# Optimization experiments

Measured on AMD Instinct MI355X. Metric: run time of the kernel, lower is better.

The kernel has to match this reference:

```python
import jax, jax.numpy as jnp
import numpy as np

N_NODES = 100000
N_EDGES = 1600000
N_FEAT = 512
HEADS = 8
F_HEAD = 8
HIDDEN = HEADS * F_HEAD  # 64
N_CLASSES = 40
NEG_SLOPE = 0.2


def setup_inputs() -> dict:
    key = jax.random.key(0)
    ks = jax.random.split(key, 10)
    x = jax.random.normal(ks[0], (N_NODES, N_FEAT), dtype=jnp.float32)
    edge_index = jax.random.randint(ks[1], (2, N_EDGES), 0, N_NODES, dtype=jnp.int32)
    s1 = 1.0 / np.sqrt(N_FEAT)
    s2 = 1.0 / np.sqrt(HIDDEN)
    return {
        "x": x,
        "edge_index": edge_index,
        "W1": jax.random.normal(ks[2], (N_FEAT, HIDDEN), dtype=jnp.float32) * s1,
        "att_src1": jax.random.normal(ks[3], (HEADS, F_HEAD), dtype=jnp.float32) * 0.1,
        "att_dst1": jax.random.normal(ks[4], (HEADS, F_HEAD), dtype=jnp.float32) * 0.1,
        "b1": jnp.zeros((HIDDEN,), dtype=jnp.float32),
        "W2": jax.random.normal(ks[5], (HIDDEN, N_CLASSES), dtype=jnp.float32) * s2,
        "att_src2": jax.random.normal(ks[6], (1, N_CLASSES), dtype=jnp.float32) * 0.1,
        "att_dst2": jax.random.normal(ks[7], (1, N_CLASSES), dtype=jnp.float32) * 0.1,
        "b2": jnp.zeros((N_CLASSES,), dtype=jnp.float32),
    }


def _gat_conv(x, src, dst, W, att_src, att_dst, bias, heads, f_out, concat):
    """PyG GATConv (v1). src/dst already include self-loops.
    x: [N, F_in]; W: [F_in, heads*f_out]; att_*: [heads, f_out]; bias: [heads*f_out] or [f_out]."""
    N = x.shape[0]
    h = (x @ W).reshape(N, heads, f_out)              # [N, H, F]
    a_src = jnp.sum(h * att_src[None], axis=-1)        # [N, H]
    a_dst = jnp.sum(h * att_dst[None], axis=-1)        # [N, H]
    e = jax.nn.leaky_relu(a_src[src] + a_dst[dst], NEG_SLOPE)  # [E, H]
    # segment softmax over incoming edges per destination node
    m = jax.ops.segment_max(e, dst, num_segments=N)    # [N, H]
    ex = jnp.exp(e - m[dst])
    denom = jax.ops.segment_sum(ex, dst, num_segments=N)
    alpha = ex / (denom[dst] + 1e-16)                  # [E, H]
    msg = h[src] * alpha[:, :, None]                   # [E, H, F]
    out = jax.ops.segment_sum(msg, dst, num_segments=N)  # [N, H, F]
    if concat:
        out = out.reshape(N, heads * f_out)
    else:
        out = out.mean(axis=1)
    return out + bias


def reference(x, edge_index, W1, att_src1, att_dst1, b1, W2, att_src2, att_dst2, b2):
    N = x.shape[0]
    loops = jnp.arange(N, dtype=edge_index.dtype)
    src = jnp.concatenate([edge_index[0], loops])
    dst = jnp.concatenate([edge_index[1], loops])
    # dropout layers are identity in eval mode
    h = _gat_conv(x, src, dst, W1, att_src1, att_dst1, b1, HEADS, F_HEAD, True)
    h = jax.nn.elu(h)
    out = _gat_conv(h, src, dst, W2, att_src2, att_dst2, b2, 1, N_CLASSES, False)
    return out
```

## Files before the change

### kernel.cpp

```cpp
#include <hip/hip_runtime.h>
#include <math.h>

#define N_NODES   100000
#define N_EDGES   1600000
#define E_TOT     (N_EDGES + N_NODES)
#define N_FEAT    512
#define HEADS     8
#define F_HEAD    8
#define HIDDEN    64
#define N_CLASSES 40

#define BSHIFT    9
#define NBUCK     196
#define SC_NBLK   256
#define SC_CHUNK  ((E_TOT + SC_NBLK - 1) / SC_NBLK)

#define CT        5

typedef __attribute__((ext_vector_type(8))) short short8_t;
typedef __attribute__((ext_vector_type(4))) float f32x4;
typedef _Float16 half_t;
typedef __attribute__((ext_vector_type(8))) _Float16 h16x8;

__device__ inline void f2bf2(float x, unsigned short& h, unsigned short& l) {
  union { float f; unsigned u; } a; a.f = x;
  unsigned rh = a.u + 0x7FFFu + ((a.u >> 16) & 1u);
  unsigned short hv = (unsigned short)(rh >> 16);
  union { unsigned u; float f; } hf; hf.u = ((unsigned)hv) << 16;
  union { float f; unsigned u; } b; b.f = x - hf.f;
  unsigned rl = b.u + 0x7FFFu + ((b.u >> 16) & 1u);
  h = hv;
  l = (unsigned short)(rl >> 16);
}

__device__ inline void cvt8(const float4& v0, const float4& v1, short8_t& hi, short8_t& lo) {
  float v[8] = {v0.x, v0.y, v0.z, v0.w, v1.x, v1.y, v1.z, v1.w};
#pragma unroll
  for (int e = 0; e < 8; ++e) {
    unsigned short hh, ll;
    f2bf2(v[e], hh, ll);
    hi[e] = (short)hh;
    lo[e] = (short)ll;
  }
}


__global__ __launch_bounds__(256) void k_bhist(const int* __restrict__ ei,
                                               int* __restrict__ ghT) {
  __shared__ int h[NBUCK];
  int b = blockIdx.x, t = threadIdx.x;
  for (int i = t; i < NBUCK; i += 256) h[i] = 0;
  __syncthreads();
  int e0 = b * SC_CHUNK;
  int e1 = e0 + SC_CHUNK; if (e1 > E_TOT) e1 = E_TOT;
  for (int e = e0 + t; e < e1; e += 256) {
    int dst = (e < N_EDGES) ? ei[N_EDGES + e] : (e - N_EDGES);
    atomicAdd(&h[dst >> BSHIFT], 1);
  }
  __syncthreads();
  for (int i = t; i < NBUCK; i += 256) ghT[i * SC_NBLK + b] = h[i];
}

__global__ __launch_bounds__(256) void k_scan1(int* __restrict__ ghT,
                                               int* __restrict__ btot) {
  __shared__ int red[256];
  int k = blockIdx.x, t = threadIdx.x;
  int v = ghT[k * SC_NBLK + t];
  red[t] = v;
  __syncthreads();
  for (int off = 1; off < 256; off <<= 1) {
    int add = (t >= off) ? red[t - off] : 0;
    __syncthreads();
    red[t] += add;
    __syncthreads();
  }
  ghT[k * SC_NBLK + t] = red[t] - v;
  if (t == 255) btot[k] = red[255];
}

__global__ __launch_bounds__(256) void k_scan2(const int* __restrict__ btot,
                                               int* __restrict__ bbase) {
  __shared__ int red[256];
  int t = threadIdx.x;
  int v = (t < NBUCK) ? btot[t] : 0;
  red[t] = v;
  __syncthreads();
  for (int off = 1; off < 256; off <<= 1) {
    int add = (t >= off) ? red[t - off] : 0;
    __syncthreads();
    red[t] += add;
    __syncthreads();
  }
  if (t < NBUCK) bbase[t] = red[t] - v;
  if (t == NBUCK - 1) bbase[NBUCK] = red[t];
}

__global__ __launch_bounds__(256) void k_bscatter(const int* __restrict__ ei,
                                                  const int* __restrict__ ghT,
                                                  const int* __restrict__ bbase,
                                                  unsigned* __restrict__ ebuf) {
  __shared__ int offs[256];
  __shared__ int cnt[256];
  int b = blockIdx.x, t = threadIdx.x;
  offs[t] = (t < NBUCK) ? (ghT[t * SC_NBLK + b] + bbase[t]) : 0;
  cnt[t] = 0;
  __syncthreads();
  int e0 = b * SC_CHUNK;
  int e1 = e0 + SC_CHUNK; if (e1 > E_TOT) e1 = E_TOT;
  for (int e = e0 + t; e < e1; e += 256) {
    int src, dst;
    if (e < N_EDGES) { src = ei[e]; dst = ei[N_EDGES + e]; }
    else             { src = e - N_EDGES; dst = src; }
    int k = dst >> BSHIFT;
    int r = atomicAdd(&cnt[k], 1);
    ebuf[offs[k] + r] = (unsigned)src | ((unsigned)(dst & 511) << 17);
  }
}

__global__ __launch_bounds__(256) void k_fine(const unsigned* __restrict__ ebuf,
                                              const int* __restrict__ bbase,
                                              int* __restrict__ rowp,
                                              int* __restrict__ ssrc) {
  __shared__ int cnt[512];
  __shared__ int red[256];
  __shared__ int cur[512];
  int k = blockIdx.x, t = threadIdx.x;
  int base = bbase[k], end = bbase[k + 1];
  cnt[t] = 0; cnt[t + 256] = 0;
  __syncthreads();
  for (int i = base + t; i < end; i += 256) atomicAdd(&cnt[ebuf[i] >> 17], 1);
  __syncthreads();
  int c0 = cnt[2 * t], c1 = cnt[2 * t + 1];
  int s = c0 + c1;
  red[t] = s;
  __syncthreads();
  for (int off = 1; off < 256; off <<= 1) {
    int add = (t >= off) ? red[t - off] : 0;
    __syncthreads();
    red[t] += add;
    __syncthreads();
  }
  int excl = red[t] - s;
  int p0 = base + excl;
  int p1 = p0 + c0;
  cur[2 * t] = p0; cur[2 * t + 1] = p1;
  int node = (k << BSHIFT) + 2 * t;
  if (node < N_NODES)     rowp[node]     = p0;
  if (node + 1 < N_NODES) rowp[node + 1] = p1;
  if (k == NBUCK - 1 && t == 0) rowp[N_NODES] = E_TOT;
  __syncthreads();
  for (int i = base + t; i < end; i += 256) {
    unsigned p = ebuf[i];
    int pos = atomicAdd(&cur[p >> 17], 1);
    ssrc[pos] = (int)(p & 0x1FFFFu);
  }
}


__global__ void k_wprep(const float* __restrict__ W1, const float* __restrict__ att_src1,
                        const float* __restrict__ att_dst1, short* __restrict__ w1fh,
                        short* __restrict__ w1fl) {
  int idx = blockIdx.x * blockDim.x + threadIdx.x;
  if (idx < N_FEAT * HIDDEN) {
    int e    = idx & 7;
    int lane = (idx >> 3) & 63;
    int ct   = (idx >> 9) & 3;
    int ks   = idx >> 11;
    int col = ct * 16 + (lane & 15);
    int k   = ks * 32 + (lane >> 4) * 8 + e;
    unsigned short h, l;
    f2bf2(W1[k * HIDDEN + col], h, l);
    int didx = ((ks * CT + ct) * 64 + lane) * 8 + e;
    w1fh[didx] = (short)h;
    w1fl[didx] = (short)l;
  } else if (idx < N_FEAT * HIDDEN + N_FEAT * 16) {
    int i2 = idx - N_FEAT * HIDDEN;
    int c = i2 & 15;
    int k = i2 >> 4;
    int cc = c & 7;
    const float* att = (c < 8) ? att_src1 : att_dst1;
    float v = 0.f;
#pragma unroll
    for (int f = 0; f < 8; ++f) v = fmaf(W1[k * HIDDEN + cc * 8 + f], att[cc * 8 + f], v);
    unsigned short h, l;
    f2bf2(v, h, l);
    int lane = ((k >> 3) & 3) * 16 + c;
    int ks = k >> 5, e = k & 7;
    int didx = ((ks * CT + 4) * 64 + lane) * 8 + e;
    w1fh[didx] = (short)h;
    w1fl[didx] = (short)l;
  }
}


__global__ __launch_bounds__(256) void k_gemm1(const float* __restrict__ x,
                                               const short* __restrict__ w1fh,
                                               const short* __restrict__ w1fl,
                                               half_t* __restrict__ h1h,
                                               half_t* __restrict__ a_srch,
                                               float* __restrict__ a_dst1) {
  int t = threadIdx.x;
  int w = t >> 6, l = t & 63;
  int n0 = blockIdx.x * 128 + w * 32;
  int r0 = l & 15;
  int kq8 = (l >> 4) * 8;
  const float* pA = x + (size_t)(n0 + r0) * N_FEAT + kq8;
  const float* pB = x + (size_t)(n0 + 16 + r0) * N_FEAT + kq8;
  bool vA = (n0 + r0) < N_NODES;
  bool vB = (n0 + 16 + r0) < N_NODES;

  f32x4 acc[2][CT];
#pragma unroll
  for (int i = 0; i < 2; ++i)
#pragma unroll
    for (int j = 0; j < CT; ++j) acc[i][j] = (f32x4){0.f, 0.f, 0.f, 0.f};

#pragma unroll 2
  for (int gks = 0; gks < 16; ++gks) {
    int boff = gks * (CT * 512) + l * 8;
    short8_t bh[CT], bl[CT];
#pragma unroll
    for (int ct = 0; ct < CT; ++ct) {
      bh[ct] = *(const short8_t*)(w1fh + boff + ct * 512);
      bl[ct] = *(const short8_t*)(w1fl + boff + ct * 512);
    }
    float4 a0 = make_float4(0.f, 0.f, 0.f, 0.f), a1 = a0, c0 = a0, c1 = a0;
    if (vA) {
      const float4* p = (const float4*)(pA + gks * 32);
      a0 = p[0]; a1 = p[1];
    }
    if (vB) {
      const float4* p = (const float4*)(pB + gks * 32);
      c0 = p[0]; c1 = p[1];
    }
    short8_t ahA, alA, ahB, alB;
    cvt8(a0, a1, ahA, alA);
    cvt8(c0, c1, ahB, alB);
#pragma unroll
    for (int ct = 0; ct < CT; ++ct) {
      acc[0][ct] = __builtin_amdgcn_mfma_f32_16x16x32_bf16(ahA, bh[ct], acc[0][ct], 0, 0, 0);
      acc[0][ct] = __builtin_amdgcn_mfma_f32_16x16x32_bf16(ahA, bl[ct], acc[0][ct], 0, 0, 0);
      acc[0][ct] = __builtin_amdgcn_mfma_f32_16x16x32_bf16(alA, bh[ct], acc[0][ct], 0, 0, 0);
      acc[1][ct] = __builtin_amdgcn_mfma_f32_16x16x32_bf16(ahB, bh[ct], acc[1][ct], 0, 0, 0);
      acc[1][ct] = __builtin_amdgcn_mfma_f32_16x16x32_bf16(ahB, bl[ct], acc[1][ct], 0, 0, 0);
      acc[1][ct] = __builtin_amdgcn_mfma_f32_16x16x32_bf16(alB, bh[ct], acc[1][ct], 0, 0, 0);
    }
  }
#pragma unroll
  for (int rtl = 0; rtl < 2; ++rtl) {
    int rbase = n0 + rtl * 16 + (l >> 4) * 4;
    int col0 = l & 15;
#pragma unroll
    for (int ct = 0; ct < 4; ++ct) {
      int col = ct * 16 + col0;
#pragma unroll
      for (int r = 0; r < 4; ++r) {
        int node = rbase + r;
        if (node < N_NODES) h1h[(size_t)node * HIDDEN + col] = (half_t)acc[rtl][ct][r];
      }
    }
#pragma unroll
    for (int r = 0; r < 4; ++r) {
      int node = rbase + r;
      if (node < N_NODES) {
        float v = acc[rtl][4][r];
        if (col0 < 8) a_srch[(size_t)node * 8 + col0] = (half_t)v;
        else          a_dst1[(size_t)node * 8 + (col0 - 8)] = v;
      }
    }
  }
}


__global__ __launch_bounds__(256) void k_edge1(const int* __restrict__ rowp,
                                               const int* __restrict__ ssrc,
                                               const half_t* __restrict__ a_srch,
                                               const float* __restrict__ a_dst,
                                               const half_t* __restrict__ h1h,
                                               const float* __restrict__ b1,
                                               const float* __restrict__ W2,
                                               const float* __restrict__ att_src2,
                                               const float* __restrict__ att_dst2,
                                               half_t* __restrict__ h2h,
                                               float* __restrict__ a_src2,
                                               float* __restrict__ a_dst2) {
  __shared__ __align__(16) float w2s[HIDDEN * N_CLASSES];
  __shared__ float as2s[N_CLASSES], ad2s[N_CLASSES];
  __shared__ half_t exsh[4][64 * 9];
  __shared__ int   srcs[4][64];
  __shared__ float orow[4][64];
  int t = threadIdx.x;
  for (int i = t; i < HIDDEN * N_CLASSES; i += 256) w2s[i] = W2[i];
  if (t < N_CLASSES) { as2s[t] = att_src2[t]; ad2s[t] = att_dst2[t]; }
  __syncthreads();

  int wv = t >> 6, lane = t & 63;
  int node = __builtin_amdgcn_readfirstlane(blockIdx.x * 4 + wv);
  int s0 = __builtin_amdgcn_readfirstlane(rowp[node]);
  int s1 = __builtin_amdgcn_readfirstlane(rowp[node + 1]);

  float ad[8];
  {
    float4 d0 = *(const float4*)(a_dst + (size_t)node * 8);
    float4 d1 = *(const float4*)(a_dst + (size_t)node * 8 + 4);
    ad[0] = d0.x; ad[1] = d0.y; ad[2] = d0.z; ad[3] = d0.w;
    ad[4] = d1.x; ad[5] = d1.y; ad[6] = d1.z; ad[7] = d1.w;
  }
  float ac0 = 0.f, ac1 = 0.f, ac2 = 0.f, ac3 = 0.f;
  float ds0 = 0.f, ds1 = 0.f, ds2 = 0.f, ds3 = 0.f;
  int hof = lane >> 3;

  for (int base = s0; base < s1; base += 64) {
    int cn = s1 - base;
    cn = cn > 64 ? 64 : cn;
    asm volatile("" ::: "memory");
    if (lane < cn) {
      int sid = ssrc[base + lane];
      h16x8 Av = *(const h16x8*)(a_srch + (size_t)sid * 8);
      srcs[wv][lane] = sid;
#pragma unroll
      for (int h = 0; h < 8; ++h) {
        float e = (float)Av[h] + ad[h];
        e = e > 0.f ? e : 0.2f * e;
        exsh[wv][lane * 9 + h] = (half_t)__expf(e);
      }
    }
    asm volatile("s_waitcnt lgkmcnt(0)" ::: "memory");
    int j = 0;
    for (; j + 8 <= cn; j += 8) {
      float e0 = (float)exsh[wv][j * 9 + hof];
      float e1 = (float)exsh[wv][(j + 1) * 9 + hof];
      float e2 = (float)exsh[wv][(j + 2) * 9 + hof];
      float e3 = (float)exsh[wv][(j + 3) * 9 + hof];
      float e4 = (float)exsh[wv][(j + 4) * 9 + hof];
      float e5 = (float)exsh[wv][(j + 5) * 9 + hof];
      float e6 = (float)exsh[wv][(j + 6) * 9 + hof];
      float e7 = (float)exsh[wv][(j + 7) * 9 + hof];
      int sj0 = __builtin_amdgcn_readfirstlane(srcs[wv][j]);
      int sj1 = __builtin_amdgcn_readfirstlane(srcs[wv][j + 1]);
      int sj2 = __builtin_amdgcn_readfirstlane(srcs[wv][j + 2]);
      int sj3 = __builtin_amdgcn_readfirstlane(srcs[wv][j + 3]);
      int sj4 = __builtin_amdgcn_readfirstlane(srcs[wv][j + 4]);
      int sj5 = __builtin_amdgcn_readfirstlane(srcs[wv][j + 5]);
      int sj6 = __builtin_amdgcn_readfirstlane(srcs[wv][j + 6]);
      int sj7 = __builtin_amdgcn_readfirstlane(srcs[wv][j + 7]);
      float g0 = (float)(h1h + (size_t)sj0 * HIDDEN)[lane];
      float g1 = (float)(h1h + (size_t)sj1 * HIDDEN)[lane];
      float g2 = (float)(h1h + (size_t)sj2 * HIDDEN)[lane];
      float g3 = (float)(h1h + (size_t)sj3 * HIDDEN)[lane];
      float g4 = (float)(h1h + (size_t)sj4 * HIDDEN)[lane];
      float g5 = (float)(h1h + (size_t)sj5 * HIDDEN)[lane];
      float g6 = (float)(h1h + (size_t)sj6 * HIDDEN)[lane];
      float g7 = (float)(h1h + (size_t)sj7 * HIDDEN)[lane];
      ac0 = fmaf(e0, g0, ac0);  ds0 += e0;
      ac1 = fmaf(e1, g1, ac1);  ds1 += e1;
      ac2 = fmaf(e2, g2, ac2);  ds2 += e2;
      ac3 = fmaf(e3, g3, ac3);  ds3 += e3;
      ac0 = fmaf(e4, g4, ac0);  ds0 += e4;
      ac1 = fmaf(e5, g5, ac1);  ds1 += e5;
      ac2 = fmaf(e6, g6, ac2);  ds2 += e6;
      ac3 = fmaf(e7, g7, ac3);  ds3 += e7;
    }
    for (; j + 4 <= cn; j += 4) {
      float e0 = (float)exsh[wv][j * 9 + hof];
      float e1 = (float)exsh[wv][(j + 1) * 9 + hof];
      float e2 = (float)exsh[wv][(j + 2) * 9 + hof];
      float e3 = (float)exsh[wv][(j + 3) * 9 + hof];
      int sj0 = __builtin_amdgcn_readfirstlane(srcs[wv][j]);
      int sj1 = __builtin_amdgcn_readfirstlane(srcs[wv][j + 1]);
      int sj2 = __builtin_amdgcn_readfirstlane(srcs[wv][j + 2]);
      int sj3 = __builtin_amdgcn_readfirstlane(srcs[wv][j + 3]);
      float g0 = (float)(h1h + (size_t)sj0 * HIDDEN)[lane];
      float g1 = (float)(h1h + (size_t)sj1 * HIDDEN)[lane];
      float g2 = (float)(h1h + (size_t)sj2 * HIDDEN)[lane];
      float g3 = (float)(h1h + (size_t)sj3 * HIDDEN)[lane];
      ac0 = fmaf(e0, g0, ac0);  ds0 += e0;
      ac1 = fmaf(e1, g1, ac1);  ds1 += e1;
      ac2 = fmaf(e2, g2, ac2);  ds2 += e2;
      ac3 = fmaf(e3, g3, ac3);  ds3 += e3;
    }
    for (; j < cn; ++j) {
      float e0 = (float)exsh[wv][j * 9 + hof];
      int sj0 = __builtin_amdgcn_readfirstlane(srcs[wv][j]);
      ac0 = fmaf(e0, (float)(h1h + (size_t)sj0 * HIDDEN)[lane], ac0);
      ds0 += e0;
    }
  }
  float accv = (ac0 + ac1) + (ac2 + ac3);
  float dsum = (ds0 + ds1) + (ds2 + ds3);
  float o = accv / (dsum + 1e-16f);
  o += b1[lane];
  o = o > 0.f ? o : expm1f(o);
  orow[wv][lane] = o;
  asm volatile("s_waitcnt lgkmcnt(0)" ::: "memory");

  float hacc = 0.f;
  if (lane < N_CLASSES) {
#pragma unroll 16
    for (int k = 0; k < HIDDEN; ++k)
      hacc = fmaf(orow[wv][k], w2s[k * N_CLASSES + lane], hacc);
  }
  float pas = (lane < N_CLASSES) ? hacc * as2s[lane] : 0.f;
  float pad = (lane < N_CLASSES) ? hacc * ad2s[lane] : 0.f;
#pragma unroll
  for (int off = 1; off < 64; off <<= 1) {
    pas += __shfl_xor(pas, off);
    pad += __shfl_xor(pad, off);
  }
  if (lane < N_CLASSES) h2h[(size_t)node * N_CLASSES + lane] = (half_t)hacc;
  if (lane == 0) { a_src2[node] = pas; a_dst2[node] = pad; }
}


__global__ __launch_bounds__(256) void k_edge2(const int* __restrict__ rowp,
                                               const int* __restrict__ ssrc,
                                               const float* __restrict__ a_src,
                                               const float* __restrict__ a_dst,
                                               const half_t* __restrict__ h2h,
                                               const float* __restrict__ b2,
                                               float* __restrict__ out) {
  __shared__ float exs[4][64];
  __shared__ int   srcs[4][64];
  int t = threadIdx.x;
  int wv = t >> 6, lane = t & 63;
  int node = __builtin_amdgcn_readfirstlane(blockIdx.x * 4 + wv);
  int s0 = __builtin_amdgcn_readfirstlane(rowp[node]);
  int s1 = __builtin_amdgcn_readfirstlane(rowp[node + 1]);

  float adv = a_dst[node];
  float ac0 = 0.f, ac1 = 0.f, ac2 = 0.f, ac3 = 0.f;
  float ds0 = 0.f, ds1 = 0.f, ds2 = 0.f, ds3 = 0.f;
  bool act = lane < N_CLASSES;

  for (int base = s0; base < s1; base += 64) {
    int cn = s1 - base;
    cn = cn > 64 ? 64 : cn;
    asm volatile("" ::: "memory");
    if (lane < cn) {
      int sid = ssrc[base + lane];
      float e = a_src[sid] + adv;
      e = e > 0.f ? e : 0.2f * e;
      srcs[wv][lane] = sid;
      exs[wv][lane] = __expf(e);
    }
    asm volatile("s_waitcnt lgkmcnt(0)" ::: "memory");
    int j = 0;
    for (; j + 8 <= cn; j += 8) {
      float e0 = exs[wv][j],     e1 = exs[wv][j + 1];
      float e2 = exs[wv][j + 2], e3 = exs[wv][j + 3];
      float e4 = exs[wv][j + 4], e5 = exs[wv][j + 5];
      float e6 = exs[wv][j + 6], e7 = exs[wv][j + 7];
      int sj0 = __builtin_amdgcn_readfirstlane(srcs[wv][j]);
      int sj1 = __builtin_amdgcn_readfirstlane(srcs[wv][j + 1]);
      int sj2 = __builtin_amdgcn_readfirstlane(srcs[wv][j + 2]);
      int sj3 = __builtin_amdgcn_readfirstlane(srcs[wv][j + 3]);
      int sj4 = __builtin_amdgcn_readfirstlane(srcs[wv][j + 4]);
      int sj5 = __builtin_amdgcn_readfirstlane(srcs[wv][j + 5]);
      int sj6 = __builtin_amdgcn_readfirstlane(srcs[wv][j + 6]);
      int sj7 = __builtin_amdgcn_readfirstlane(srcs[wv][j + 7]);
      ds0 += e0; ds1 += e1; ds2 += e2; ds3 += e3;
      ds0 += e4; ds1 += e5; ds2 += e6; ds3 += e7;
      if (act) {
        float g0 = (float)(h2h + (size_t)sj0 * N_CLASSES)[lane];
        float g1 = (float)(h2h + (size_t)sj1 * N_CLASSES)[lane];
        float g2 = (float)(h2h + (size_t)sj2 * N_CLASSES)[lane];
        float g3 = (float)(h2h + (size_t)sj3 * N_CLASSES)[lane];
        float g4 = (float)(h2h + (size_t)sj4 * N_CLASSES)[lane];
        float g5 = (float)(h2h + (size_t)sj5 * N_CLASSES)[lane];
        float g6 = (float)(h2h + (size_t)sj6 * N_CLASSES)[lane];
        float g7 = (float)(h2h + (size_t)sj7 * N_CLASSES)[lane];
        ac0 = fmaf(e0, g0, ac0); ac1 = fmaf(e1, g1, ac1);
        ac2 = fmaf(e2, g2, ac2); ac3 = fmaf(e3, g3, ac3);
        ac0 = fmaf(e4, g4, ac0); ac1 = fmaf(e5, g5, ac1);
        ac2 = fmaf(e6, g6, ac2); ac3 = fmaf(e7, g7, ac3);
      }
    }
    for (; j < cn; ++j) {
      float e0 = exs[wv][j];
      int sj0 = __builtin_amdgcn_readfirstlane(srcs[wv][j]);
      ds0 += e0;
      if (act) ac0 = fmaf(e0, (float)(h2h + (size_t)sj0 * N_CLASSES)[lane], ac0);
    }
  }
  float accv = (ac0 + ac1) + (ac2 + ac3);
  float dsum = (ds0 + ds1) + (ds2 + ds3);
  if (act)
    out[(size_t)node * N_CLASSES + lane] = accv / (dsum + 1e-16f) + b2[lane];
}


extern "C" void kernel_launch(void* const* d_in, const int* in_sizes, int n_in,
                              void* d_out, int out_size, void* d_ws, size_t ws_size,
                              hipStream_t stream) {
  const float* x        = (const float*)d_in[0];
  const int*   ei       = (const int*)d_in[1];
  const float* W1       = (const float*)d_in[2];
  const float* att_src1 = (const float*)d_in[3];
  const float* att_dst1 = (const float*)d_in[4];
  const float* b1       = (const float*)d_in[5];
  const float* W2       = (const float*)d_in[6];
  const float* att_src2 = (const float*)d_in[7];
  const float* att_dst2 = (const float*)d_in[8];
  const float* b2       = (const float*)d_in[9];
  float* out = (float*)d_out;

  char* w = (char*)d_ws;
  half_t* h1h    = (half_t*)(w);
  half_t* h2h    = (half_t*)(w + 12800000);
  half_t* a_srch = (half_t*)(w + 20800000);
  float* a_dst1  = (float*)(w + 22400000);
  int*   rowp    = (int*)(w + 25600000);
  int*   ssrc    = (int*)(w + 26000128);
  short* w1fh    = (short*)(w + 32800128);
  short* w1fl    = (short*)(w + 32882048);
  float* a_src2  = (float*)(w + 32964096);
  float* a_dst2  = (float*)(w + 33364096);
  int*   btot    = (int*)(w + 33764096);
  int*   bbase   = (int*)(w + 33765120);
  unsigned* ebuf = (unsigned*)(w);
  int*   ghT     = (int*)(w + 12800000);

  k_wprep<<<(N_FEAT * HIDDEN + N_FEAT * 16 + 255) / 256, 256, 0, stream>>>(
      W1, att_src1, att_dst1, w1fh, w1fl);
  k_bhist<<<SC_NBLK, 256, 0, stream>>>(ei, ghT);
  k_scan1<<<NBUCK, 256, 0, stream>>>(ghT, btot);
  k_scan2<<<1, 256, 0, stream>>>(btot, bbase);
  k_bscatter<<<SC_NBLK, 256, 0, stream>>>(ei, ghT, bbase, ebuf);
  k_fine<<<NBUCK, 256, 0, stream>>>(ebuf, bbase, rowp, ssrc);

  k_gemm1<<<(N_NODES + 127) / 128, 256, 0, stream>>>(x, w1fh, w1fl, h1h, a_srch, a_dst1);
  k_edge1<<<N_NODES / 4, 256, 0, stream>>>(rowp, ssrc, a_srch, a_dst1, h1h, b1,
                                           W2, att_src2, att_dst2, h2h, a_src2, a_dst2);

  k_edge2<<<N_NODES / 4, 256, 0, stream>>>(rowp, ssrc, a_src2, a_dst2, h2h, b2, out);
}
```

Before: 290.7 us.

## Split layer-1 aggregation per head and move second GEMM into separate kernel

The fused edge-aggregation plus W2 projection kernel is split in two. A per-head aggregation kernel uses one wave per (node, head) pair, with lanes covering 8 edges by 8 features. A separate per-node GEMM2 kernel then computes h2 and the layer-2 attention scalars from an fp16 intermediate buffer. The aim is more parallelism and more gathers in flight during aggregation. The cost is 8x redundant reads of edge indices and attention logits, narrower 16-byte scattered gathers, an extra intermediate write and read, and one more kernel launch.

```diff
diff --git a/kernel.cpp b/kernel.cpp
--- a/kernel.cpp
+++ b/kernel.cpp
@@ -272,12 +272,70 @@
 }
 
 
-__global__ __launch_bounds__(256) void k_edge1(const int* __restrict__ rowp,
-                                               const int* __restrict__ ssrc,
-                                               const half_t* __restrict__ a_srch,
-                                               const float* __restrict__ a_dst,
-                                               const half_t* __restrict__ h1h,
-                                               const float* __restrict__ b1,
+__global__ __launch_bounds__(256) void k_edge1h(const int* __restrict__ rowp,
+                                                const int* __restrict__ ssrc,
+                                                const half_t* __restrict__ a_srch,
+                                                const float* __restrict__ a_dst1,
+                                                const half_t* __restrict__ h1h,
+                                                const float* __restrict__ b1,
+                                                half_t* __restrict__ out1h) {
+  __shared__ float exs[4][64];
+  __shared__ int   srcs[4][64];
+  int t = threadIdx.x;
+  int wv = t >> 6, lane = t & 63;
+  int head = blockIdx.x & 7;
+  int nb   = blockIdx.x >> 3;
+  int node = __builtin_amdgcn_readfirstlane(nb * 4 + wv);
+  int s0 = __builtin_amdgcn_readfirstlane(rowp[node]);
+  int s1 = __builtin_amdgcn_readfirstlane(rowp[node + 1]);
+  int es = lane >> 3, cg = lane & 7;
+  float adh = a_dst1[node * 8 + head];
+  const half_t* hbase = h1h + head * 8 + cg;
+
+  float ac0 = 0.f, ac1 = 0.f, ds0 = 0.f, ds1 = 0.f;
+
+  for (int base = s0; base < s1; base += 64) {
+    int cn = s1 - base;
+    cn = cn > 64 ? 64 : cn;
+    asm volatile("" ::: "memory");
+    int sid = 0;
+    float ex = 0.f;
+    if (lane < cn) {
+      sid = ssrc[base + lane];
+      float e = (float)a_srch[(size_t)sid * 8 + head] + adh;
+      e = e > 0.f ? e : 0.2f * e;
+      ex = __expf(e);
+    }
+    srcs[wv][lane] = sid;
+    exs[wv][lane] = ex;
+    asm volatile("s_waitcnt lgkmcnt(0)" ::: "memory");
+#pragma unroll
+    for (int jj = 0; jj < 8; jj += 2) {
+      int i0 = jj * 8 + es;
+      int i1 = i0 + 8;
+      int sj0 = srcs[wv][i0];
+      int sj1 = srcs[wv][i1];
+      float e0 = exs[wv][i0];
+      float e1 = exs[wv][i1];
+      float g0 = (float)hbase[(size_t)sj0 * HIDDEN];
+      float g1 = (float)hbase[(size_t)sj1 * HIDDEN];
+      ac0 = fmaf(e0, g0, ac0);  ds0 += e0;
+      ac1 = fmaf(e1, g1, ac1);  ds1 += e1;
+    }
+  }
+  float acc = ac0 + ac1;
+  float dsum = ds0 + ds1;
+  acc += __shfl_xor(acc, 8);  acc += __shfl_xor(acc, 16);  acc += __shfl_xor(acc, 32);
+  dsum += __shfl_xor(dsum, 8); dsum += __shfl_xor(dsum, 16); dsum += __shfl_xor(dsum, 32);
+  if (es == 0) {
+    float o = acc / (dsum + 1e-16f) + b1[head * 8 + cg];
+    o = o > 0.f ? o : expm1f(o);
+    out1h[(size_t)node * HIDDEN + head * 8 + cg] = (half_t)o;
+  }
+}
+
+
+__global__ __launch_bounds__(256) void k_gemm2(const half_t* __restrict__ out1h,
                                                const float* __restrict__ W2,
                                                const float* __restrict__ att_src2,
                                                const float* __restrict__ att_dst2,
@@ -285,130 +343,44 @@
                                                float* __restrict__ a_src2,
                                                float* __restrict__ a_dst2) {
   __shared__ __align__(16) float w2s[HIDDEN * N_CLASSES];
-  __shared__ float as2s[N_CLASSES], ad2s[N_CLASSES];
-  __shared__ half_t exsh[4][64 * 9];
-  __shared__ int   srcs[4][64];
-  __shared__ float orow[4][64];
+  __shared__ float as2[N_CLASSES], ad2[N_CLASSES];
   int t = threadIdx.x;
   for (int i = t; i < HIDDEN * N_CLASSES; i += 256) w2s[i] = W2[i];
-  if (t < N_CLASSES) { as2s[t] = att_src2[t]; ad2s[t] = att_dst2[t]; }
-  __syncthreads();
-
-  int wv = t >> 6, lane = t & 63;
-  int node = __builtin_amdgcn_readfirstlane(blockIdx.x * 4 + wv);
-  int s0 = __builtin_amdgcn_readfirstlane(rowp[node]);
-  int s1 = __builtin_amdgcn_readfirstlane(rowp[node + 1]);
-
-  float ad[8];
-  {
-    float4 d0 = *(const float4*)(a_dst + (size_t)node * 8);
-    float4 d1 = *(const float4*)(a_dst + (size_t)node * 8 + 4);
-    ad[0] = d0.x; ad[1] = d0.y; ad[2] = d0.z; ad[3] = d0.w;
-    ad[4] = d1.x; ad[5] = d1.y; ad[6] = d1.z; ad[7] = d1.w;
-  }
-  float ac0 = 0.f, ac1 = 0.f, ac2 = 0.f, ac3 = 0.f;
-  float ds0 = 0.f, ds1 = 0.f, ds2 = 0.f, ds3 = 0.f;
-  int hof = lane >> 3;
-
-  for (int base = s0; base < s1; base += 64) {
-    int cn = s1 - base;
-    cn = cn > 64 ? 64 : cn;
-    asm volatile("" ::: "memory");
-    if (lane < cn) {
-      int sid = ssrc[base + lane];
-      h16x8 Av = *(const h16x8*)(a_srch + (size_t)sid * 8);
-      srcs[wv][lane] = sid;
-#pragma unroll
-      for (int h = 0; h < 8; ++h) {
-        float e = (float)Av[h] + ad[h];
-        e = e > 0.f ? e : 0.2f * e;
-        exsh[wv][lane * 9 + h] = (half_t)__expf(e);
+  if (t < N_CLASSES) { as2[t] = att_src2[t]; ad2[t] = att_dst2[t]; }
+  __syncthreads();
+  int node = blockIdx.x * 256 + t;
+  if (node >= N_NODES) return;
+  const h16x8* rp = (const h16x8*)(out1h + (size_t)node * HIDDEN);
+  float acc[N_CLASSES];
+#pragma unroll
+  for (int c = 0; c < N_CLASSES; ++c) acc[c] = 0.f;
+  for (int k8 = 0; k8 < 8; ++k8) {
+    h16x8 rv = rp[k8];
+#pragma unroll
+    for (int kk = 0; kk < 8; ++kk) {
+      float r = (float)rv[kk];
+      const float* wrow = &w2s[(k8 * 8 + kk) * N_CLASSES];
+#pragma unroll
+      for (int c4 = 0; c4 < 10; ++c4) {
+        float4 wvv = *(const float4*)(wrow + c4 * 4);
+        acc[c4 * 4 + 0] = fmaf(r, wvv.x, acc[c4 * 4 + 0]);
+        acc[c4 * 4 + 1] = fmaf(r, wvv.y, acc[c4 * 4 + 1]);
+        acc[c4 * 4 + 2] = fmaf(r, wvv.z, acc[c4 * 4 + 2]);
+        acc[c4 * 4 + 3] = fmaf(r, wvv.w, acc[c4 * 4 + 3]);
       }
     }
-    asm volatile("s_waitcnt lgkmcnt(0)" ::: "memory");
-    int j = 0;
-    for (; j + 8 <= cn; j += 8) {
-      float e0 = (float)exsh[wv][j * 9 + hof];
-      float e1 = (float)exsh[wv][(j + 1) * 9 + hof];
-      float e2 = (float)exsh[wv][(j + 2) * 9 + hof];
-      float e3 = (float)exsh[wv][(j + 3) * 9 + hof];
-      float e4 = (float)exsh[wv][(j + 4) * 9 + hof];
-      float e5 = (float)exsh[wv][(j + 5) * 9 + hof];
-      float e6 = (float)exsh[wv][(j + 6) * 9 + hof];
-      float e7 = (float)exsh[wv][(j + 7) * 9 + hof];
-      int sj0 = __builtin_amdgcn_readfirstlane(srcs[wv][j]);
-      int sj1 = __builtin_amdgcn_readfirstlane(srcs[wv][j + 1]);
-      int sj2 = __builtin_amdgcn_readfirstlane(srcs[wv][j + 2]);
-      int sj3 = __builtin_amdgcn_readfirstlane(srcs[wv][j + 3]);
-      int sj4 = __builtin_amdgcn_readfirstlane(srcs[wv][j + 4]);
-      int sj5 = __builtin_amdgcn_readfirstlane(srcs[wv][j + 5]);
-      int sj6 = __builtin_amdgcn_readfirstlane(srcs[wv][j + 6]);
-      int sj7 = __builtin_amdgcn_readfirstlane(srcs[wv][j + 7]);
-      float g0 = (float)(h1h + (size_t)sj0 * HIDDEN)[lane];
-      float g1 = (float)(h1h + (size_t)sj1 * HIDDEN)[lane];
-      float g2 = (float)(h1h + (size_t)sj2 * HIDDEN)[lane];
-      float g3 = (float)(h1h + (size_t)sj3 * HIDDEN)[lane];
-      float g4 = (float)(h1h + (size_t)sj4 * HIDDEN)[lane];
-      float g5 = (float)(h1h + (size_t)sj5 * HIDDEN)[lane];
-      float g6 = (float)(h1h + (size_t)sj6 * HIDDEN)[lane];
-      float g7 = (float)(h1h + (size_t)sj7 * HIDDEN)[lane];
-      ac0 = fmaf(e0, g0, ac0);  ds0 += e0;
-      ac1 = fmaf(e1, g1, ac1);  ds1 += e1;
-      ac2 = fmaf(e2, g2, ac2);  ds2 += e2;
-      ac3 = fmaf(e3, g3, ac3);  ds3 += e3;
-      ac0 = fmaf(e4, g4, ac0);  ds0 += e4;
-      ac1 = fmaf(e5, g5, ac1);  ds1 += e5;
-      ac2 = fmaf(e6, g6, ac2);  ds2 += e6;
-      ac3 = fmaf(e7, g7, ac3);  ds3 += e7;
-    }
-    for (; j + 4 <= cn; j += 4) {
-      float e0 = (float)exsh[wv][j * 9 + hof];
-      float e1 = (float)exsh[wv][(j + 1) * 9 + hof];
-      float e2 = (float)exsh[wv][(j + 2) * 9 + hof];
-      float e3 = (float)exsh[wv][(j + 3) * 9 + hof];
-      int sj0 = __builtin_amdgcn_readfirstlane(srcs[wv][j]);
-      int sj1 = __builtin_amdgcn_readfirstlane(srcs[wv][j + 1]);
-      int sj2 = __builtin_amdgcn_readfirstlane(srcs[wv][j + 2]);
-      int sj3 = __builtin_amdgcn_readfirstlane(srcs[wv][j + 3]);
-      float g0 = (float)(h1h + (size_t)sj0 * HIDDEN)[lane];
-      float g1 = (float)(h1h + (size_t)sj1 * HIDDEN)[lane];
-      float g2 = (float)(h1h + (size_t)sj2 * HIDDEN)[lane];
-      float g3 = (float)(h1h + (size_t)sj3 * HIDDEN)[lane];
-      ac0 = fmaf(e0, g0, ac0);  ds0 += e0;
-      ac1 = fmaf(e1, g1, ac1);  ds1 += e1;
-      ac2 = fmaf(e2, g2, ac2);  ds2 += e2;
-      ac3 = fmaf(e3, g3, ac3);  ds3 += e3;
-    }
-    for (; j < cn; ++j) {
-      float e0 = (float)exsh[wv][j * 9 + hof];
-      int sj0 = __builtin_amdgcn_readfirstlane(srcs[wv][j]);
-      ac0 = fmaf(e0, (float)(h1h + (size_t)sj0 * HIDDEN)[lane], ac0);
-      ds0 += e0;
-    }
-  }
-  float accv = (ac0 + ac1) + (ac2 + ac3);
-  float dsum = (ds0 + ds1) + (ds2 + ds3);
-  float o = accv / (dsum + 1e-16f);
-  o += b1[lane];
-  o = o > 0.f ? o : expm1f(o);
-  orow[wv][lane] = o;
-  asm volatile("s_waitcnt lgkmcnt(0)" ::: "memory");
-
-  float hacc = 0.f;
-  if (lane < N_CLASSES) {
-#pragma unroll 16
-    for (int k = 0; k < HIDDEN; ++k)
-      hacc = fmaf(orow[wv][k], w2s[k * N_CLASSES + lane], hacc);
-  }
-  float pas = (lane < N_CLASSES) ? hacc * as2s[lane] : 0.f;
-  float pad = (lane < N_CLASSES) ? hacc * ad2s[lane] : 0.f;
-#pragma unroll
-  for (int off = 1; off < 64; off <<= 1) {
-    pas += __shfl_xor(pas, off);
-    pad += __shfl_xor(pad, off);
-  }
-  if (lane < N_CLASSES) h2h[(size_t)node * N_CLASSES + lane] = (half_t)hacc;
-  if (lane == 0) { a_src2[node] = pas; a_dst2[node] = pad; }
+  }
+  float as = 0.f, ad = 0.f;
+#pragma unroll
+  for (int c = 0; c < N_CLASSES; ++c) {
+    as = fmaf(acc[c], as2[c], as);
+    ad = fmaf(acc[c], ad2[c], ad);
+  }
+  half_t* hp = h2h + (size_t)node * N_CLASSES;
+#pragma unroll
+  for (int c = 0; c < N_CLASSES; ++c) hp[c] = (half_t)acc[c];
+  a_src2[node] = as;
+  a_dst2[node] = ad;
 }
 
 
@@ -517,6 +489,7 @@
   float* a_dst2  = (float*)(w + 33364096);
   int*   btot    = (int*)(w + 33764096);
   int*   bbase   = (int*)(w + 33765120);
+  half_t* out1h  = (half_t*)(w + 33766400);
   unsigned* ebuf = (unsigned*)(w);
   int*   ghT     = (int*)(w + 12800000);
 
@@ -529,8 +502,9 @@
   k_fine<<<NBUCK, 256, 0, stream>>>(ebuf, bbase, rowp, ssrc);
 
   k_gemm1<<<(N_NODES + 127) / 128, 256, 0, stream>>>(x, w1fh, w1fl, h1h, a_srch, a_dst1);
-  k_edge1<<<N_NODES / 4, 256, 0, stream>>>(rowp, ssrc, a_srch, a_dst1, h1h, b1,
-                                           W2, att_src2, att_dst2, h2h, a_src2, a_dst2);
-
+  k_edge1h<<<(N_NODES / 4) * 8, 256, 0, stream>>>(rowp, ssrc, a_srch, a_dst1, h1h, b1, out1h);
+
+  k_gemm2<<<(N_NODES + 255) / 256, 256, 0, stream>>>(out1h, W2, att_src2, att_dst2,
+                                                     h2h, a_src2, a_dst2);
   k_edge2<<<N_NODES / 4, 256, 0, stream>>>(rowp, ssrc, a_src2, a_dst2, h2h, b2, out);
 }
```

After: 489.5 us. 68.4% more time.
